# Performance work log

Measured on AMD Instinct MI355X. Metric: run time of the kernel, lower is better.

## Reference

```python
import jax, jax.numpy as jnp
import numpy as np

T, D_IN, D_OUT, HEADS, FREQ = 2048, 1024, 1024, 8, 10000
DH = D_OUT // HEADS


def absolute_pos(t, d, freq):
    # AP[pos, 2i] = sin(pos / freq**(2i/d)), AP[pos, 2i+1] = cos(...); t even -> all cols filled
    pos = jnp.arange(t, dtype=jnp.float32)[:, None]            # [T,1]
    i = jnp.arange(t // 2, dtype=jnp.float32)[None, :]         # [1,T/2]
    angle = pos / (freq ** (2.0 * i / d))                      # [T,T/2]
    return jnp.stack([jnp.sin(angle), jnp.cos(angle)], axis=-1).reshape(t, t)


def setup_inputs() -> dict:
    key = jax.random.key(0)
    ks = jax.random.split(key, 6)
    s = 0.02
    return {
        "x": jax.random.normal(ks[0], (T, D_IN), jnp.float32),
        "Wq": jax.random.normal(ks[1], (HEADS, DH, D_IN), jnp.float32) * s,
        "Wk": jax.random.normal(ks[2], (HEADS, DH, D_IN), jnp.float32) * s,
        "Wv": jax.random.normal(ks[3], (HEADS, DH, D_IN), jnp.float32) * s,
        "Wout2": jax.random.normal(ks[4], (DH, DH + 2), jnp.float32) * s,
        "Wout": jax.random.normal(ks[5], (D_IN, D_OUT), jnp.float32) * s,
    }


def reference(x, Wq, Wk, Wv, Wout2, Wout):
    t = x.shape[0]
    # diversity = 1 - cosine similarity (F.normalize with eps=1e-12)
    x_unit = x / jnp.maximum(jnp.linalg.norm(x, axis=1, keepdims=True), 1e-12)
    diversity = 1.0 - x_unit @ x_unit.T                        # [T,T]

    # all heads vectorized; torch Linear weight is [out,in] -> x @ W.T
    Q = jnp.einsum('td,hed->hte', x, Wq)                       # [H,T,DH]
    K = jnp.einsum('td,hed->hte', x, Wk)
    V = jnp.einsum('td,hed->hte', x, Wv)

    AP = absolute_pos(t, D_IN, FREQ)                           # [T,T]
    energies = jnp.einsum('hte,hse->hts', Q, K) + AP           # [H,T,T]

    att = jax.nn.softmax(energies, axis=-1)
    logp = jax.nn.log_softmax(energies, axis=-1)
    entropy = -(att * logp).sum(-1) / np.float32(np.log(t))    # [H,T]
    entropy = entropy / jnp.maximum(jnp.abs(entropy).sum(-1, keepdims=True), 1e-12)

    # dep_factor[j] broadcast over rows: masked[i,j] = dep[j]*att[i,j]
    dep = (diversity[None] * att).sum(-1) / diversity.sum(-1)[None]  # [H,T]
    att_win = att + dep[:, None, :] * att                      # [H,T,T]

    # dropout(p=0.5) treated as identity (eval mode)
    y = jnp.einsum('hts,hse->hte', att_win, V)                 # [H,T,DH]

    chars = jax.lax.stop_gradient(jnp.stack([entropy, dep], axis=-1))  # [H,T,2]
    y_s = jnp.einsum('htf,of->hto', jnp.concatenate([y, chars], axis=-1), Wout2)  # [H,T,DH]

    y_cat = jnp.transpose(y_s, (1, 0, 2)).reshape(t, D_OUT)    # cat heads along feature dim
    out = y_cat @ Wout.T                                       # [T,D_IN]
    return out, att_win[-1]
```

## Files before the change

kernel.cpp:

```cpp
#include <hip/hip_runtime.h>
#include <math.h>

#define TT  2048
#define NH  8
#define DH  128
#define LNT 7.6246189861593985f

typedef unsigned short ushort_t;
typedef __bf16 bf16x8 __attribute__((ext_vector_type(8)));
typedef _Float16 f16x8 __attribute__((ext_vector_type(8)));
typedef float f32x4 __attribute__((ext_vector_type(4)));
typedef unsigned int uintx4 __attribute__((ext_vector_type(4)));

#define MFMA16(a, b, c)  __builtin_amdgcn_mfma_f32_16x16x32_bf16(a, b, c, 0, 0, 0)
#define MFMA16F(a, b, c) __builtin_amdgcn_mfma_f32_16x16x32_f16(a, b, c, 0, 0, 0)

#define GLL(gp, lp) __builtin_amdgcn_global_load_lds(                        \
    (const __attribute__((address_space(1))) void*)(gp),                     \
    (__attribute__((address_space(3))) void*)(lp), 16, 0, 0)

__device__ __forceinline__ bf16x8 ld8(const ushort_t* p) {
  uintx4 v = *(const uintx4*)p;
  return __builtin_bit_cast(bf16x8, v);
}
__device__ __forceinline__ f16x8 ld8f(const ushort_t* p) {
  uintx4 v = *(const uintx4*)p;
  return __builtin_bit_cast(f16x8, v);
}
__device__ __forceinline__ ushort_t f2bf(float x) {
  unsigned u = __float_as_uint(x);
  return (ushort_t)((u + 0x7fffu + ((u >> 16) & 1u)) >> 16);
}
__device__ __forceinline__ float bf2f(ushort_t b) {
  return __uint_as_float(((unsigned)b) << 16);
}
__device__ __forceinline__ ushort_t f2h(float x) {
  return __builtin_bit_cast(ushort_t, (_Float16)x);
}
__device__ __forceinline__ float h2f(ushort_t b) {
  return (float)__builtin_bit_cast(_Float16, b);
}


enum : size_t {
  F_XF   = 0u,
  F_UF   = 1048576u,
  F_QF   = 2097152u,
  F_KF   = 3145728u,
  F_VBF  = 4194304u,
  F_VT   = 5242880u,
  F_YCF  = 6291456u,
  F_WCAT = 7340032u,
  F_WOF  = 9437184u,
  F_DIVS = 9961472u,
  F_LST  = 9979904u,
  F_ENTR = 9996288u,
  F_ENT  = 10012672u,
  F_DEP  = 10029056u,
  F_W2F  = 10307584u,
  F_APH  = 10485760u,
  F_C    = 12582912u,
  F_LP   = 6291456u,
  F_SAP  = 6422528u,
  F_SCP  = 6553600u,
  F_E    = 16777216u,
  F_YPALL= 33554432u,
  F_YSH  = 2097152u,
};

__device__ __forceinline__ float blockReduceSum256(float v) {
  __shared__ float sh[4];
  #pragma unroll
  for (int m = 1; m < 64; m <<= 1) v += __shfl_xor(v, m, 64);
  if ((threadIdx.x & 63) == 0) sh[threadIdx.x >> 6] = v;
  __syncthreads();
  float r = sh[0] + sh[1] + sh[2] + sh[3];
  __syncthreads();
  return r;
}

__global__ __launch_bounds__(256) void k_pre(
    const float* __restrict__ x, const float* __restrict__ Wq,
    const float* __restrict__ Wk, const float* __restrict__ Wv,
    const float* __restrict__ Wo, const float* __restrict__ W2,
    ushort_t* __restrict__ xf, ushort_t* __restrict__ Wcat,
    ushort_t* __restrict__ Wof, ushort_t* __restrict__ W2f,
    ushort_t* __restrict__ Uf, float* __restrict__ divsum) {
  int b = blockIdx.x;
  if (b < 4192) {
    int i = b * 256 + threadIdx.x;
    if (i < 1048576) {
      const float* src; ushort_t* dst; int j;
      if (i < 262144)       { src = Wq; dst = Wcat;           j = i; }
      else if (i < 524288)  { src = Wk; dst = Wcat + 1048576; j = i - 262144; }
      else if (i < 786432)  { src = Wv; dst = Wcat + 2097152; j = i - 524288; }
      else                  { src = Wo; dst = Wof;            j = i - 786432; }
      float4 v = ((const float4*)src)[j];
      uint2 w;
      w.x = (unsigned)f2h(v.x) | ((unsigned)f2h(v.y) << 16);
      w.y = (unsigned)f2h(v.z) | ((unsigned)f2h(v.w) << 16);
      ((uint2*)dst)[j] = w;
    } else {
      int idx = i - 1048576;
      int o = idx / 192, c = idx % 192;
      W2f[idx] = (c < 130) ? f2h(W2[o * 130 + c]) : (ushort_t)0;
    }
  } else if (b < 6240) {
    int t = b - 4192;
    const float* xr = x + (size_t)t * 1024;
    float ss = 0.f;
    for (int d = threadIdx.x; d < 1024; d += 256) { float v = xr[d]; ss += v * v; }
    ss = blockReduceSum256(ss);
    float inv = 1.f / fmaxf(sqrtf(ss), 1e-12f);
    for (int d = threadIdx.x; d < 1024; d += 256) {
      float v = xr[d];
      Uf[(size_t)t * 1024 + d] = f2h(v * inv);
      xf[(size_t)t * 1024 + d] = f2h(v);
    }
  } else {
    int idx = (b - 6240) * 256 + threadIdx.x;
    if (idx < TT) divsum[idx] = (float)TT;
  }
}

template <int MODE>
__device__ __forceinline__ void gemm_tile(
    ushort_t* As, ushort_t* Bs,
    const ushort_t* A, const ushort_t* B,
    float* Df, ushort_t* Dh,
    int M, int N, int K, int m0, int n0) {
  int tid = threadIdx.x, lane = tid & 63, w = tid >> 6;
  int l15 = lane & 15, lg = lane >> 4;
  int wr = w >> 1, wc = w & 1;

  const ushort_t* ga[4];
  const ushort_t* gb[4];
  ushort_t* la[4];
  ushort_t* lb[4];
  #pragma unroll
  for (int j = 0; j < 4; j++) {
    int u = (4 * w + j) * 64 + lane;
    int row = u >> 3;
    int kc8 = (u & 7) ^ (row & 7);
    ga[j] = A + (size_t)(m0 + row) * K + kc8 * 8;
    gb[j] = B + (size_t)(n0 + row) * K + kc8 * 8;
    la[j] = As + (4 * w + j) * 512;
    lb[j] = Bs + (4 * w + j) * 512;
  }

  f32x4 acc[4][4];
  #pragma unroll
  for (int i = 0; i < 4; i++)
    #pragma unroll
    for (int ct = 0; ct < 4; ct++) acc[i][ct] = (f32x4)0.f;

  for (int k0 = 0; k0 < K; k0 += 64) {
    __syncthreads();
    #pragma unroll
    for (int j = 0; j < 4; j++) {
      GLL(ga[j] + k0, la[j]);
      GLL(gb[j] + k0, lb[j]);
    }
    __syncthreads();
    #pragma unroll
    for (int kc = 0; kc < 2; kc++) {
      f16x8 af[4], bfr[4];
      #pragma unroll
      for (int i = 0; i < 4; i++) {
        int ra = wr * 64 + i * 16 + l15;
        af[i] = ld8f(As + (ra * 8 + ((kc * 4 + lg) ^ (ra & 7))) * 8);
        int rb = wc * 64 + i * 16 + l15;
        bfr[i] = ld8f(Bs + (rb * 8 + ((kc * 4 + lg) ^ (rb & 7))) * 8);
      }
      #pragma unroll
      for (int i = 0; i < 4; i++)
        #pragma unroll
        for (int ct = 0; ct < 4; ct++)
          acc[i][ct] = MFMA16F(af[i], bfr[ct], acc[i][ct]);
    }
  }
  if (MODE == 7) {
    #pragma unroll
    for (int i = 0; i < 4; i++) {
      float rs[4] = {0.f, 0.f, 0.f, 0.f};
      #pragma unroll
      for (int ct = 0; ct < 4; ct++) {
        size_t tile_t = (size_t)(m0 + wr * 64 + i * 16) >> 4;
        size_t tile_s = (size_t)(n0 + wc * 64 + ct * 16) >> 4;
        uint2 wv;
        wv.x = (unsigned)f2bf(acc[i][ct][0]) | ((unsigned)f2bf(acc[i][ct][1]) << 16);
        wv.y = (unsigned)f2bf(acc[i][ct][2]) | ((unsigned)f2bf(acc[i][ct][3]) << 16);
        *(uint2*)(Dh + (tile_t * (size_t)(N >> 4) + tile_s) * 256 + lg * 64 + l15 * 4) = wv;
        rs[0] += acc[i][ct][0]; rs[1] += acc[i][ct][1];
        rs[2] += acc[i][ct][2]; rs[3] += acc[i][ct][3];
      }
      #pragma unroll
      for (int r = 0; r < 4; r++) {
        float s = rs[r];
        s += __shfl_xor(s, 1, 64); s += __shfl_xor(s, 2, 64);
        s += __shfl_xor(s, 4, 64); s += __shfl_xor(s, 8, 64);
        if (l15 == 0)
          atomicAdd(&Df[m0 + wr * 64 + i * 16 + lg * 4 + r], -s);
      }
    }
    if (m0 != n0) {
      #pragma unroll
      for (int ct = 0; ct < 4; ct++) {
        float cs = 0.f;
        #pragma unroll
        for (int i = 0; i < 4; i++)
          #pragma unroll
          for (int r = 0; r < 4; r++) cs += acc[i][ct][r];
        cs += __shfl_xor(cs, 16, 64);
        cs += __shfl_xor(cs, 32, 64);
        if (lane < 16)
          atomicAdd(&Df[n0 + wc * 64 + ct * 16 + l15], -cs);
      }
      #pragma unroll
      for (int i = 0; i < 4; i++) {
        #pragma unroll
        for (int ct = 0; ct < 4; ct++) {
          size_t mbase = (((size_t)(n0 + wc * 64 + ct * 16) >> 4) * (size_t)(N >> 4)
                          + ((size_t)(m0 + wr * 64 + i * 16) >> 4)) * 256;
          #pragma unroll
          for (int r = 0; r < 4; r++)
            Dh[mbase + (l15 >> 2) * 64 + (lg * 4 + r) * 4 + (l15 & 3)] =
                f2bf(acc[i][ct][r]);
        }
      }
    }
  }
}

template <int MODE>
__device__ __forceinline__ void gemm64(
    ushort_t* As0, ushort_t* As1, ushort_t* Bs0, ushort_t* Bs1,
    const ushort_t* A, const ushort_t* B,
    float* Df, ushort_t* Dh,
    ushort_t* Dq, ushort_t* Dk, ushort_t* Dv,
    int N, int K, int m0, int n0) {
  int tid = threadIdx.x, lane = tid & 63, w = tid >> 6;
  int l15 = lane & 15, lg = lane >> 4;
  int wc = w;

  const ushort_t* gaA[2];
  int laOff[2];
  #pragma unroll
  for (int j = 0; j < 2; j++) {
    int u = (2 * w + j) * 64 + lane;
    int row = u >> 3;
    int kc8 = (u & 7) ^ (row & 7);
    gaA[j] = A + (size_t)(m0 + row) * K + kc8 * 8;
    laOff[j] = (2 * w + j) * 512;
  }
  const ushort_t* gb[4];
  int lbOff[4];
  #pragma unroll
  for (int j = 0; j < 4; j++) {
    int u = (4 * w + j) * 64 + lane;
    int row = u >> 3;
    int kc8 = (u & 7) ^ (row & 7);
    gb[j] = B + (size_t)(n0 + row) * K + kc8 * 8;
    lbOff[j] = (4 * w + j) * 512;
  }

  f32x4 acc[4][2];
  #pragma unroll
  for (int i = 0; i < 4; i++)
    #pragma unroll
    for (int ct = 0; ct < 2; ct++) acc[i][ct] = (f32x4)0.f;

  #pragma unroll
  for (int j = 0; j < 2; j++) GLL(gaA[j], As0 + laOff[j]);
  #pragma unroll
  for (int j = 0; j < 4; j++) GLL(gb[j], Bs0 + lbOff[j]);
  __syncthreads();

  int cur = 0;
  for (int k0 = 0; k0 < K; k0 += 64) {
    ushort_t* Ac = cur ? As1 : As0;
    ushort_t* Bc = cur ? Bs1 : Bs0;
    int k1 = k0 + 64;
    if (k1 < K) {
      ushort_t* An = cur ? As0 : As1;
      ushort_t* Bn = cur ? Bs0 : Bs1;
      #pragma unroll
      for (int j = 0; j < 2; j++) GLL(gaA[j] + k1, An + laOff[j]);
      #pragma unroll
      for (int j = 0; j < 4; j++) GLL(gb[j] + k1, Bn + lbOff[j]);
    }
    #pragma unroll
    for (int kc = 0; kc < 2; kc++) {
      f16x8 af[4], bfr[2];
      #pragma unroll
      for (int i = 0; i < 4; i++) {
        int ra = i * 16 + l15;
        af[i] = ld8f(Ac + (ra * 8 + ((kc * 4 + lg) ^ (ra & 7))) * 8);
      }
      #pragma unroll
      for (int ct = 0; ct < 2; ct++) {
        int rb = wc * 32 + ct * 16 + l15;
        bfr[ct] = ld8f(Bc + (rb * 8 + ((kc * 4 + lg) ^ (rb & 7))) * 8);
      }
      #pragma unroll
      for (int i = 0; i < 4; i++)
        #pragma unroll
        for (int ct = 0; ct < 2; ct++)
          acc[i][ct] = MFMA16F(af[i], bfr[ct], acc[i][ct]);
    }
    __syncthreads();
    cur ^= 1;
  }
  #pragma unroll
  for (int i = 0; i < 4; i++) {
    #pragma unroll
    for (int ct = 0; ct < 2; ct++) {
      #pragma unroll
      for (int r = 0; r < 4; r++) {
        size_t mm = m0 + i * 16 + lg * 4 + r;
        size_t nn = n0 + wc * 32 + ct * 16 + l15;
        float v = acc[i][ct][r];
        if (MODE == 0) Df[mm * N + nn] = v;
        if (MODE == 3) {
          if (nn < 1024) Dq[mm * 1024 + nn] = f2h(v);
          else if (nn < 2048) Dk[mm * 1024 + nn - 1024] = f2h(v);
          else Dv[mm * 1024 + nn - 2048] = f2bf(v);
        }
        if (MODE == 4) {
          size_t hh = mm >> 11, tt2 = mm & 2047;
          Dh[tt2 * 1024 + hh * 128 + nn] = f2h(v);
        }
      }
    }
  }
}

template <int MODE>
__global__ __launch_bounds__(256) void k_gemm64(
    const ushort_t* __restrict__ A, const ushort_t* __restrict__ B,
    float* __restrict__ Df, ushort_t* __restrict__ Dh,
    int N, int K) {
  __shared__ __align__(16) ushort_t SA[2][64 * 64];
  __shared__ __align__(16) ushort_t SB[2][128 * 64];
  gemm64<MODE>(SA[0], SA[1], SB[0], SB[1], A, B, Df, Dh,
               nullptr, nullptr, nullptr,
               N, K, blockIdx.y * 64, blockIdx.x * 128);
}

__global__ __launch_bounds__(256) void k_cqkv(
    const ushort_t* __restrict__ Uf, const ushort_t* __restrict__ xf,
    const ushort_t* __restrict__ Wcat,
    ushort_t* __restrict__ Cf, ushort_t* __restrict__ Qf,
    ushort_t* __restrict__ Kf, ushort_t* __restrict__ Vbf,
    float* __restrict__ divsum, ushort_t* __restrict__ APf) {
  __shared__ __align__(16) ushort_t SA[2][64 * 64];
  __shared__ __align__(16) ushort_t SB[2][128 * 64];
  int bid = blockIdx.x;
  if (bid < 136) {
    int rem = bid, bt = 0;
    while (rem >= 16 - bt) { rem -= 16 - bt; ++bt; }
    int bs = bt + rem;
    gemm_tile<7>(&SA[0][0], &SB[0][0], Uf, Uf, divsum, Cf,
                 TT, TT, 1024, bt * 128, bs * 128);
  } else if (bid < 904) {
    int b = bid - 136;
    gemm64<3>(SA[0], SA[1], SB[0], SB[1], xf, Wcat, nullptr, nullptr,
              Qf, Kf, Vbf, 3072, 1024, (b / 24) * 64, (b % 24) * 128);
  } else {
    int bb = bid - 904;
    int tile_t = bb >> 4, sub = bb & 15;
    int base = sub * 2048;
    for (int u0 = threadIdx.x; u0 < 2048; u0 += 256) {
      int u = base + u0;
      int tile_s = u >> 8, slot = u & 255;
      int lg = slot >> 6, l15 = (slot >> 2) & 15, r = slot & 3;
      int t = tile_t * 16 + lg * 4 + r;
      int s = tile_s * 16 + l15;
      int i = s >> 1;
      float invf = __expf((float)i * -0.017988946039016016f);
      float ang = (float)t * invf;
      APf[(size_t)tile_t * 32768 + u] = f2h((s & 1) ? cosf(ang) : sinf(ang));
    }
  }
}

__global__ __launch_bounds__(512, 4) void k_phase1m(
    const ushort_t* __restrict__ Qf, const ushort_t* __restrict__ Kf,
    const ushort_t* __restrict__ APf, const ushort_t* __restrict__ Cf,
    ushort_t* __restrict__ Ef,
    float* __restrict__ Lp, float* __restrict__ sap, float* __restrict__ scp) {
  int h = blockIdx.y, z = blockIdx.z;
  int tid = threadIdx.x, lane = tid & 63, w = tid >> 6;
  int l15 = lane & 15, lg = lane >> 4;
  int rowbase = blockIdx.x * 128 + w * 16;
  int s_begin = z * 256, s_end = s_begin + 256;
  __shared__ __align__(16) ushort_t Ks[64 * 128];

  f16x8 q[4];
  {
    const ushort_t* qp = Qf + (size_t)(rowbase + l15) * 1024 + h * DH + lg * 8;
    #pragma unroll
    for (int kc = 0; kc < 4; kc++) q[kc] = ld8f(qp + kc * 32);
  }
  const ushort_t* apb = APf + (size_t)(rowbase >> 4) * 32768 + lane * 4;
  const ushort_t* cfb = Cf  + (size_t)(rowbase >> 4) * 32768 + lane * 4;
  ushort_t* eb = Ef + ((size_t)(h * 128 + (rowbase >> 4)) * 128) * 256 + lane * 4;

  int n0 = w * 128 + lane;
  int sr0 = n0 >> 4, su0 = n0 & 15, sr1 = sr0 + 4;
  int wo0 = sr0 * 128 + ((su0 ^ (sr0 & 7)) * 8);
  int wo1 = sr1 * 128 + ((su0 ^ (sr1 & 7)) * 8);
  const ushort_t* kg0 = Kf + (size_t)sr0 * 1024 + h * DH + su0 * 8;
  const ushort_t* kg1 = Kf + (size_t)sr1 * 1024 + h * DH + su0 * 8;

  float Lv[4], sae[4], snc[4];
  #pragma unroll
  for (int r = 0; r < 4; r++) { Lv[r] = 0.f; sae[r] = 0.f; snc[r] = 0.f; }

  uintx4 ka = *(const uintx4*)(kg0 + (size_t)s_begin * 1024);
  uintx4 kb = *(const uintx4*)(kg1 + (size_t)s_begin * 1024);

  for (int s0 = s_begin; s0 < s_end; s0 += 64) {
    int ts0 = s0 >> 4;
    f32x4 acc[4];
    float cc[4][4];
    #pragma unroll
    for (int ct = 0; ct < 4; ct++) {
      uint2 ap2 = *(const uint2*)(apb + (size_t)(ts0 + ct) * 256);
      uint2 c2  = *(const uint2*)(cfb + (size_t)(ts0 + ct) * 256);
      acc[ct][0] = h2f((ushort_t)(ap2.x & 0xffffu));
      acc[ct][1] = h2f((ushort_t)(ap2.x >> 16));
      acc[ct][2] = h2f((ushort_t)(ap2.y & 0xffffu));
      acc[ct][3] = h2f((ushort_t)(ap2.y >> 16));
      cc[ct][0] = bf2f((ushort_t)(c2.x & 0xffffu));
      cc[ct][1] = bf2f((ushort_t)(c2.x >> 16));
      cc[ct][2] = bf2f((ushort_t)(c2.y & 0xffffu));
      cc[ct][3] = bf2f((ushort_t)(c2.y >> 16));
    }
    __syncthreads();
    *(uintx4*)(Ks + wo0) = ka;
    *(uintx4*)(Ks + wo1) = kb;
    int s1 = s0 + 64;
    if (s1 < s_end) {
      ka = *(const uintx4*)(kg0 + (size_t)s1 * 1024);
      kb = *(const uintx4*)(kg1 + (size_t)s1 * 1024);
    }
    __syncthreads();
    #pragma unroll
    for (int ct = 0; ct < 4; ct++) {
      int row = ct * 16 + l15, rb = row * 128, rsw = row & 7;
      #pragma unroll
      for (int kc = 0; kc < 4; kc++) {
        f16x8 b = ld8f(Ks + rb + (((kc * 4 + lg) ^ rsw) * 8));
        acc[ct] = MFMA16F(q[kc], b, acc[ct]);
      }
    }
    #pragma unroll
    for (int ct = 0; ct < 4; ct++) {
      uint2 ev;
      ev.x = (unsigned)f2h(acc[ct][0]) | ((unsigned)f2h(acc[ct][1]) << 16);
      ev.y = (unsigned)f2h(acc[ct][2]) | ((unsigned)f2h(acc[ct][3]) << 16);
      *(uint2*)(eb + (size_t)(ts0 + ct) * 256) = ev;
    }
    #pragma unroll
    for (int r = 0; r < 4; r++) {
      float e0 = acc[0][r], e1 = acc[1][r], e2 = acc[2][r], e3 = acc[3][r];
      float p0 = __expf(e0), p1 = __expf(e1), p2 = __expf(e2), p3 = __expf(e3);
      Lv[r]  += (p0 + p1) + (p2 + p3);
      sae[r] += (p0 * e0 + p1 * e1) + (p2 * e2 + p3 * e3);
      snc[r] += (p0 * cc[0][r] + p1 * cc[1][r]) + (p2 * cc[2][r] + p3 * cc[3][r]);
    }
  }
  #pragma unroll
  for (int r = 0; r < 4; r++) {
    #pragma unroll
    for (int m = 1; m < 16; m <<= 1) {
      Lv[r]  += __shfl_xor(Lv[r], m, 64);
      sae[r] += __shfl_xor(sae[r], m, 64);
      snc[r] += __shfl_xor(snc[r], m, 64);
    }
  }
  if (l15 == 0) {
    #pragma unroll
    for (int r = 0; r < 4; r++) {
      int t = rowbase + lg * 4 + r;
      size_t idx = (size_t)z * (NH * TT) + h * TT + t;
      Lp[idx] = Lv[r]; sap[idx] = sae[r]; scp[idx] = snc[r];
    }
  }
}

__global__ __launch_bounds__(256) void k_combine(
    const float* __restrict__ Lp, const float* __restrict__ sap,
    const float* __restrict__ scp, const float* __restrict__ divsum,
    float* __restrict__ Lst, float* __restrict__ entraw, float* __restrict__ dep) {
  int i = blockIdx.x * 256 + threadIdx.x;
  if (i >= NH * TT) return;
  float L = 0.f, sa = 0.f, sc = 0.f;
  #pragma unroll
  for (int c = 0; c < 8; c++) {
    size_t idx = (size_t)c * (NH * TT) + i;
    L += Lp[idx]; sa += sap[idx]; sc += scp[idx];
  }
  float logL = __logf(L);
  Lst[i] = logL;
  entraw[i] = (logL - sa / L) * (1.0f / LNT);
  int t = i & (TT - 1);
  dep[i] = (1.f - sc / L) / divsum[t];
}

__global__ __launch_bounds__(256) void k_entvp(
    const float* __restrict__ entraw, float* __restrict__ ent,
    const ushort_t* __restrict__ Vbf, const float* __restrict__ dep,
    ushort_t* __restrict__ VT) {
  __shared__ float tile[64][130];
  int b = blockIdx.x;
  if (b < 8) {
    int h = b;
    float s = 0.f;
    for (int t = threadIdx.x; t < TT; t += 256) s += fabsf(entraw[h * TT + t]);
    s = blockReduceSum256(s);
    float inv = 1.f / fmaxf(s, 1e-12f);
    for (int t = threadIdx.x; t < TT; t += 256)
      ent[h * TT + t] = entraw[h * TT + t] * inv;
  } else {
    int bb = b - 8;
    int h = bb >> 5, s0 = (bb & 31) * 64;
    int tid = threadIdx.x;
    for (int idx = tid; idx < 64 * 64; idx += 256) {
      int r = idx >> 6, c2 = (idx & 63) * 2;
      unsigned u = *(const unsigned*)&Vbf[(size_t)(s0 + r) * 1024 + h * DH + c2];
      tile[r][c2] = bf2f((ushort_t)(u & 0xffffu));
      tile[r][c2 + 1] = bf2f((ushort_t)(u >> 16));
    }
    __syncthreads();
    int e = tid >> 1, sh = (tid & 1) * 32;
    #pragma unroll
    for (int g = 0; g < 8; g++) {
      int sb = sh + g * 4;
      float v0 = tile[sb + 0][e] * (1.f + dep[h * TT + s0 + sb + 0]);
      float v1 = tile[sb + 1][e] * (1.f + dep[h * TT + s0 + sb + 1]);
      float v2 = tile[sb + 2][e] * (1.f + dep[h * TT + s0 + sb + 2]);
      float v3 = tile[sb + 3][e] * (1.f + dep[h * TT + s0 + sb + 3]);
      uint2 wv;
      wv.x = (unsigned)f2bf(v0) | ((unsigned)f2bf(v1) << 16);
      wv.y = (unsigned)f2bf(v2) | ((unsigned)f2bf(v3) << 16);
      *(uint2*)&VT[(size_t)(h * DH + e) * TT + s0 + sb] = wv;
    }
  }
}

__global__ __launch_bounds__(512, 4) void k_phase2m(
    const ushort_t* __restrict__ Ef, const ushort_t* __restrict__ VT,
    const float* __restrict__ Lst, const float* __restrict__ dep,
    ushort_t* __restrict__ ypall, float* __restrict__ out2) {
  int h = (blockIdx.y + 7) & 7;
  int z = blockIdx.z;
  int tid = threadIdx.x, lane = tid & 63, w = tid >> 6;
  int l15 = lane & 15, lg = lane >> 4;
  int rowbase = blockIdx.x * 128 + w * 16;
  bool last = (h == NH - 1);
  int s_begin = z * 256, s_end = s_begin + 256;
  ushort_t* yp = ypall + (size_t)z * 2097152;

  __shared__ __align__(16) ushort_t Vs[128 * 64];
  __shared__ __align__(16) ushort_t Pst[8][16][72];

  float ml[4];
  #pragma unroll
  for (int r = 0; r < 4; r++) ml[r] = Lst[h * TT + rowbase + lg * 4 + r];
  const ushort_t* eb = Ef + ((size_t)(h * 128 + (rowbase >> 4)) * 128) * 256 + lane * 4;

  int n0 = w * 128 + lane;
  int ve0 = n0 >> 3, vu0 = n0 & 7;
  int vwo0 = ve0 * 64 + ((vu0 ^ (ve0 & 7)) * 8);
  int vwo1 = vwo0 + 512;
  const ushort_t* vg0 = VT + (size_t)(h * DH + ve0) * TT + vu0 * 8;
  const ushort_t* vg1 = vg0 + (size_t)8 * TT;

  f32x4 yacc[8];
  #pragma unroll
  for (int et = 0; et < 8; et++) yacc[et] = (f32x4)0.f;

  uintx4 va = *(const uintx4*)(vg0 + s_begin);
  uintx4 vb = *(const uintx4*)(vg1 + s_begin);

  for (int s0 = s_begin; s0 < s_end; s0 += 64) {
    int ts0 = s0 >> 4;
    uint2 e2[4];
    #pragma unroll
    for (int ct = 0; ct < 4; ct++)
      e2[ct] = *(const uint2*)(eb + (size_t)(ts0 + ct) * 256);
    __syncthreads();
    *(uintx4*)(Vs + vwo0) = va;
    *(uintx4*)(Vs + vwo1) = vb;
    int s1 = s0 + 64;
    if (s1 < s_end) {
      va = *(const uintx4*)(vg0 + s1);
      vb = *(const uintx4*)(vg1 + s1);
    }
    __syncthreads();
    float dv[4];
    if (last) {
      #pragma unroll
      for (int ct = 0; ct < 4; ct++) dv[ct] = dep[(NH - 1) * TT + s0 + ct * 16 + l15];
    }
    #pragma unroll
    for (int ct = 0; ct < 4; ct++) {
      float e0 = h2f((ushort_t)(e2[ct].x & 0xffffu));
      float e1 = h2f((ushort_t)(e2[ct].x >> 16));
      float e3 = h2f((ushort_t)(e2[ct].y & 0xffffu));
      float e4 = h2f((ushort_t)(e2[ct].y >> 16));
      float a0 = __expf(e0 - ml[0]);
      float a1 = __expf(e1 - ml[1]);
      float a2 = __expf(e3 - ml[2]);
      float a3 = __expf(e4 - ml[3]);
      Pst[w][lg * 4 + 0][ct * 16 + l15] = f2bf(a0);
      Pst[w][lg * 4 + 1][ct * 16 + l15] = f2bf(a1);
      Pst[w][lg * 4 + 2][ct * 16 + l15] = f2bf(a2);
      Pst[w][lg * 4 + 3][ct * 16 + l15] = f2bf(a3);
      if (last) {
        float sc = 1.f + dv[ct];
        out2[(size_t)(rowbase + lg * 4 + 0) * TT + s0 + ct * 16 + l15] = a0 * sc;
        out2[(size_t)(rowbase + lg * 4 + 1) * TT + s0 + ct * 16 + l15] = a1 * sc;
        out2[(size_t)(rowbase + lg * 4 + 2) * TT + s0 + ct * 16 + l15] = a2 * sc;
        out2[(size_t)(rowbase + lg * 4 + 3) * TT + s0 + ct * 16 + l15] = a3 * sc;
      }
    }
    asm volatile("" ::: "memory");
    #pragma unroll
    for (int c = 0; c < 2; c++) {
      bf16x8 ap = *(const bf16x8*)&Pst[w][l15][c * 32 + lg * 8];
      #pragma unroll
      for (int et = 0; et < 8; et++) {
        int e = et * 16 + l15;
        bf16x8 bv = ld8(Vs + e * 64 + (((c * 4 + lg) ^ (l15 & 7)) * 8));
        yacc[et] = MFMA16(ap, bv, yacc[et]);
      }
    }
    asm volatile("" ::: "memory");
  }
  #pragma unroll
  for (int et = 0; et < 8; et++)
    #pragma unroll
    for (int r = 0; r < 4; r++)
      yp[((size_t)h * TT + rowbase + lg * 4 + r) * DH + et * 16 + l15] = f2h(yacc[et][r]);
}

__device__ __forceinline__ void acc8(const ushort_t* p, float* s) {
  uintx4 v = *(const uintx4*)p;
  #pragma unroll
  for (int q = 0; q < 4; q++) {
    s[q * 2]     += h2f((ushort_t)(v[q] & 0xffffu));
    s[q * 2 + 1] += h2f((ushort_t)(v[q] >> 16));
  }
}
__global__ __launch_bounds__(256) void k_ysum(
    const ushort_t* __restrict__ ypall,
    const float* __restrict__ ent, const float* __restrict__ dep,
    ushort_t* __restrict__ ysh) {
  int i = blockIdx.x * 256 + threadIdx.x;
  int g = i & 15, t = (i >> 4) & 2047, h = i >> 15;
  size_t src = ((size_t)h * TT + t) * DH + g * 8;
  float s[8];
  #pragma unroll
  for (int q = 0; q < 8; q++) s[q] = 0.f;
  #pragma unroll
  for (int b = 0; b < 8; b++) acc8(ypall + (size_t)b * 2097152 + src, s);
  uintx4 o;
  o[0] = (unsigned)f2h(s[0]) | ((unsigned)f2h(s[1]) << 16);
  o[1] = (unsigned)f2h(s[2]) | ((unsigned)f2h(s[3]) << 16);
  o[2] = (unsigned)f2h(s[4]) | ((unsigned)f2h(s[5]) << 16);
  o[3] = (unsigned)f2h(s[6]) | ((unsigned)f2h(s[7]) << 16);
  ushort_t* row = ysh + ((size_t)h * TT + t) * 192;
  *(uintx4*)(row + g * 8) = o;
  if (g == 0) {
    uint2 cz;
    cz.x = (unsigned)f2h(ent[h * TT + t]) | ((unsigned)f2h(dep[h * TT + t]) << 16);
    cz.y = 0u;
    *(uint2*)(row + 128) = cz;
    uint2 z2; z2.x = 0u; z2.y = 0u;
    #pragma unroll
    for (int q = 132; q < 192; q += 4) *(uint2*)(row + q) = z2;
  }
}

extern "C" void kernel_launch(void* const* d_in, const int* in_sizes, int n_in,
                              void* d_out, int out_size, void* d_ws, size_t ws_size,
                              hipStream_t stream) {
  const float* x  = (const float*)d_in[0];
  const float* Wq = (const float*)d_in[1];
  const float* Wk = (const float*)d_in[2];
  const float* Wv = (const float*)d_in[3];
  const float* W2 = (const float*)d_in[4];
  const float* Wo = (const float*)d_in[5];
  float* out  = (float*)d_out;
  float* out2 = out + (size_t)TT * 1024;
  float* ws = (float*)d_ws;

  ushort_t* xf   = (ushort_t*)(ws + F_XF);
  ushort_t* Uf   = (ushort_t*)(ws + F_UF);
  ushort_t* Qf   = (ushort_t*)(ws + F_QF);
  ushort_t* Kf   = (ushort_t*)(ws + F_KF);
  ushort_t* Vbf  = (ushort_t*)(ws + F_VBF);
  ushort_t* VT   = (ushort_t*)(ws + F_VT);
  ushort_t* ycf  = (ushort_t*)(ws + F_YCF);
  ushort_t* Wcat = (ushort_t*)(ws + F_WCAT);
  ushort_t* Wof  = (ushort_t*)(ws + F_WOF);
  ushort_t* W2f  = (ushort_t*)(ws + F_W2F);
  ushort_t* APf  = (ushort_t*)(ws + F_APH);
  ushort_t* ysh  = (ushort_t*)(ws + F_YSH);
  ushort_t* Cf   = (ushort_t*)(ws + F_C);
  ushort_t* Ef   = (ushort_t*)(ws + F_E);
  ushort_t* ypall= (ushort_t*)(ws + F_YPALL);
  float* divsum = ws + F_DIVS;
  float* Lst    = ws + F_LST;
  float* entraw = ws + F_ENTR;
  float* ent    = ws + F_ENT;
  float* dep    = ws + F_DEP;
  float* Lp     = ws + F_LP;
  float* sap    = ws + F_SAP;
  float* scp    = ws + F_SCP;

  k_pre<<<6248, 256, 0, stream>>>(x, Wq, Wk, Wv, Wo, W2,
                                  xf, Wcat, Wof, W2f, Uf, divsum);
  k_cqkv<<<2952, 256, 0, stream>>>(Uf, xf, Wcat, Cf, Qf, Kf, Vbf, divsum, APf);

  k_phase1m<<<dim3(16, NH, 8), 512, 0, stream>>>(Qf, Kf, APf, Cf, Ef, Lp, sap, scp);
  k_combine<<<64, 256, 0, stream>>>(Lp, sap, scp, divsum, Lst, entraw, dep);
  k_entvp<<<264, 256, 0, stream>>>(entraw, ent, Vbf, dep, VT);
  k_phase2m<<<dim3(16, NH, 8), 512, 0, stream>>>(Ef, VT, Lst, dep, ypall, out2);
  k_ysum<<<1024, 256, 0, stream>>>(ypall, ent, dep, ysh);
  k_gemm64<4><<<dim3(1, 256), 256, 0, stream>>>(ysh, W2f, nullptr, ycf, 128, 192);
  k_gemm64<0><<<dim3(8, 32), 256, 0, stream>>>(ycf, Wof, out, nullptr, 1024, 1024);
}
```

Before: 147.5 us.

## Double-buffer K tiles in phase1 and vectorize normalization and AP generation

```diff
diff --git a/kernel.cpp b/kernel.cpp
--- a/kernel.cpp
+++ b/kernel.cpp
@@ -107,16 +107,17 @@
     }
   } else if (b < 6240) {
     int t = b - 4192;
-    const float* xr = x + (size_t)t * 1024;
-    float ss = 0.f;
-    for (int d = threadIdx.x; d < 1024; d += 256) { float v = xr[d]; ss += v * v; }
+    float4 v = ((const float4*)(x + (size_t)t * 1024))[threadIdx.x];
+    float ss = v.x * v.x + v.y * v.y + v.z * v.z + v.w * v.w;
     ss = blockReduceSum256(ss);
     float inv = 1.f / fmaxf(sqrtf(ss), 1e-12f);
-    for (int d = threadIdx.x; d < 1024; d += 256) {
-      float v = xr[d];
-      Uf[(size_t)t * 1024 + d] = f2h(v * inv);
-      xf[(size_t)t * 1024 + d] = f2h(v);
-    }
+    uint2 wU, wX;
+    wU.x = (unsigned)f2h(v.x * inv) | ((unsigned)f2h(v.y * inv) << 16);
+    wU.y = (unsigned)f2h(v.z * inv) | ((unsigned)f2h(v.w * inv) << 16);
+    wX.x = (unsigned)f2h(v.x) | ((unsigned)f2h(v.y) << 16);
+    wX.y = (unsigned)f2h(v.z) | ((unsigned)f2h(v.w) << 16);
+    ((uint2*)(Uf + (size_t)t * 1024))[threadIdx.x] = wU;
+    ((uint2*)(xf + (size_t)t * 1024))[threadIdx.x] = wX;
   } else {
     int idx = (b - 6240) * 256 + threadIdx.x;
     if (idx < TT) divsum[idx] = (float)TT;
@@ -379,7 +380,7 @@
       int i = s >> 1;
       float invf = __expf((float)i * -0.017988946039016016f);
       float ang = (float)t * invf;
-      APf[(size_t)tile_t * 32768 + u] = f2h((s & 1) ? cosf(ang) : sinf(ang));
+      APf[(size_t)tile_t * 32768 + u] = f2h((s & 1) ? __cosf(ang) : __sinf(ang));
     }
   }
 }
@@ -394,7 +395,7 @@
   int l15 = lane & 15, lg = lane >> 4;
   int rowbase = blockIdx.x * 128 + w * 16;
   int s_begin = z * 256, s_end = s_begin + 256;
-  __shared__ __align__(16) ushort_t Ks[64 * 128];
+  __shared__ __align__(16) ushort_t Ks[2][64 * 128];
 
   f16x8 q[4];
   {
@@ -419,7 +420,15 @@
 
   uintx4 ka = *(const uintx4*)(kg0 + (size_t)s_begin * 1024);
   uintx4 kb = *(const uintx4*)(kg1 + (size_t)s_begin * 1024);
-
+  *(uintx4*)(Ks[0] + wo0) = ka;
+  *(uintx4*)(Ks[0] + wo1) = kb;
+  __syncthreads();
+  if (s_begin + 64 < s_end) {
+    ka = *(const uintx4*)(kg0 + (size_t)(s_begin + 64) * 1024);
+    kb = *(const uintx4*)(kg1 + (size_t)(s_begin + 64) * 1024);
+  }
+
+  int cur = 0;
   for (int s0 = s_begin; s0 < s_end; s0 += 64) {
     int ts0 = s0 >> 4;
     f32x4 acc[4];
@@ -437,21 +446,23 @@
       cc[ct][2] = bf2f((ushort_t)(c2.y & 0xffffu));
       cc[ct][3] = bf2f((ushort_t)(c2.y >> 16));
     }
-    __syncthreads();
-    *(uintx4*)(Ks + wo0) = ka;
-    *(uintx4*)(Ks + wo1) = kb;
     int s1 = s0 + 64;
     if (s1 < s_end) {
-      ka = *(const uintx4*)(kg0 + (size_t)s1 * 1024);
-      kb = *(const uintx4*)(kg1 + (size_t)s1 * 1024);
-    }
-    __syncthreads();
+      *(uintx4*)(Ks[cur ^ 1] + wo0) = ka;
+      *(uintx4*)(Ks[cur ^ 1] + wo1) = kb;
+      int s2 = s0 + 128;
+      if (s2 < s_end) {
+        ka = *(const uintx4*)(kg0 + (size_t)s2 * 1024);
+        kb = *(const uintx4*)(kg1 + (size_t)s2 * 1024);
+      }
+    }
+    const ushort_t* Kc = Ks[cur];
     #pragma unroll
     for (int ct = 0; ct < 4; ct++) {
       int row = ct * 16 + l15, rb = row * 128, rsw = row & 7;
       #pragma unroll
       for (int kc = 0; kc < 4; kc++) {
-        f16x8 b = ld8f(Ks + rb + (((kc * 4 + lg) ^ rsw) * 8));
+        f16x8 b = ld8f(Kc + rb + (((kc * 4 + lg) ^ rsw) * 8));
         acc[ct] = MFMA16F(q[kc], b, acc[ct]);
       }
     }
@@ -470,6 +481,8 @@
       sae[r] += (p0 * e0 + p1 * e1) + (p2 * e2 + p3 * e3);
       snc[r] += (p0 * cc[0][r] + p1 * cc[1][r]) + (p2 * cc[2][r] + p3 * cc[3][r]);
     }
+    __syncthreads();
+    cur ^= 1;
   }
   #pragma unroll
   for (int r = 0; r < 4; r++) {
```

Measured after the change: 142.7 us (median of 3 runs). -3.3%, faster.
